# Performance work log

Hardware: AMD Instinct MI355X
Metric: run time of the kernel (lower is better)

The kernel has to match this reference:

```python
import jax, jax.numpy as jnp
import numpy as np

N_NODES = 20000; N_EDGES = 200000
FN = 128; FE = 64; D = 128; T = 128; K = 5
H = 4; DH = D // H; N_LAYERS = 2; FF = 4 * D
B = 32768
T0 = 0.0; EPS = 1e-5


def _ln(x, s, b):
    m = jnp.mean(x, axis=-1, keepdims=True)
    v = jnp.mean(jnp.square(x - m), axis=-1, keepdims=True)
    return (x - m) / jnp.sqrt(v + EPS) * s + b


def setup_inputs() -> dict:
    key = jax.random.key(0)
    ks = jax.random.split(key, 24)
    def w(i, shape, s=0.05):
        return jax.random.normal(ks[i], shape, jnp.float32) * s
    return {
        "src": jax.random.randint(ks[0], (B,), 0, N_NODES),
        "dst": jax.random.randint(ks[1], (B,), 0, N_NODES),
        "neg": jax.random.randint(ks[2], (B,), 0, N_NODES),
        "eidx": jax.random.randint(ks[3], (B,), 0, N_EDGES),
        "ts": jax.random.uniform(ks[4], (B,), jnp.float32) * 1000.0,
        "node_feats": w(5, (N_NODES, FN), 1.0),
        "edge_feats": w(6, (N_EDGES, FE), 1.0),
        "node_lin_w": w(7, (D, FN)), "node_lin_b": jnp.zeros((D,), jnp.float32),
        "edge_lin_w": w(8, (D, FE)), "edge_lin_b": jnp.zeros((D,), jnp.float32),
        "time_w": w(9, (T,), 1.0), "time_b": w(10, (T,), 1.0),
        "tok_w": w(11, (D, 3 * D + T)), "tok_b": jnp.zeros((D,), jnp.float32),
        "qkv_w": w(12, (N_LAYERS, 3 * D, D)), "qkv_b": jnp.zeros((N_LAYERS, 3 * D), jnp.float32),
        "attn_w": w(13, (N_LAYERS, D, D)), "attn_b": jnp.zeros((N_LAYERS, D), jnp.float32),
        "ln1_s": jnp.ones((N_LAYERS, D), jnp.float32), "ln1_b": jnp.zeros((N_LAYERS, D), jnp.float32),
        "ln2_s": jnp.ones((N_LAYERS, D), jnp.float32), "ln2_b": jnp.zeros((N_LAYERS, D), jnp.float32),
        "ff1_w": w(14, (N_LAYERS, FF, D)), "ff1_b": jnp.zeros((N_LAYERS, FF), jnp.float32),
        "ff2_w": w(15, (N_LAYERS, D, FF)), "ff2_b": jnp.zeros((N_LAYERS, D), jnp.float32),
        "p1_w": w(16, (D, D)), "p1_b": jnp.zeros((D,), jnp.float32),
        "p2_w": w(17, (K, D)), "p2_b": jnp.zeros((K,), jnp.float32),
    }


def reference(src, dst, neg, eidx, ts, node_feats, edge_feats,
              node_lin_w, node_lin_b, edge_lin_w, edge_lin_b,
              time_w, time_b, tok_w, tok_b,
              qkv_w, qkv_b, attn_w, attn_b,
              ln1_s, ln1_b, ln2_s, ln2_b,
              ff1_w, ff1_b, ff2_w, ff2_b,
              p1_w, p1_b, p2_w, p2_b):
    # --- occurrence tokens: [src occs | dst occs | neg occs] = 3B tokens ---
    self_nodes = jnp.concatenate([src, dst, neg])          # [3B]
    other_nodes = jnp.concatenate([dst, src, src])         # [3B]
    eidx_all = jnp.concatenate([eidx, eidx, eidx])
    ts_all = jnp.concatenate([ts, ts, ts])
    Ntot = self_nodes.shape[0]

    base_self = node_feats[self_nodes] @ node_lin_w.T + node_lin_b    # [3B, D]
    base_other = node_feats[other_nodes] @ node_lin_w.T + node_lin_b
    edge_emb = edge_feats[eidx_all] @ edge_lin_w.T + edge_lin_b       # [3B, D]
    time_emb = jnp.cos((ts_all - T0)[:, None] * time_w[None, :] + time_b)  # [3B, T]
    x_cat = jnp.concatenate([base_self, base_other, edge_emb, time_emb], axis=-1)
    tok = jax.nn.relu(x_cat @ tok_w.T + tok_b)                        # [3B, D]

    # --- group occurrences by node, sort by time, pad (device-side) ---
    node_ids = jnp.unique(self_nodes)                      # [Nn]
    order = jnp.lexsort((ts_all, self_nodes))              # primary node, secondary time
    nodes_s = self_nodes[order]
    row_s = jnp.searchsorted(node_ids, nodes_s)            # row per sorted occ
    starts = jnp.searchsorted(nodes_s, node_ids)           # start of each group
    pos_s = jnp.arange(Ntot) - starts[row_s]               # pos within group
    node_row = jnp.zeros((Ntot,), jnp.int32).at[order].set(row_s.astype(jnp.int32))
    pos_map = jnp.zeros((Ntot,), jnp.int32).at[order].set(pos_s.astype(jnp.int32))
    seq_len = jnp.diff(jnp.concatenate([starts, jnp.array([Ntot], starts.dtype)]))
    Nn = int(node_ids.shape[0])
    Lmax = int(seq_len.max())

    x_pad = jnp.zeros((Nn, Lmax, D), tok.dtype).at[node_row, pos_map].set(tok)
    pad_mask = jnp.arange(Lmax)[None, :] >= seq_len[:, None]  # True = padded key

    # --- pre-LN TransformerEncoder (gelu, no final norm) ---
    scale = jnp.float32(1.0 / np.sqrt(DH))
    x = x_pad
    for l in range(N_LAYERS):
        h = _ln(x, ln1_s[l], ln1_b[l])
        qkv = h @ qkv_w[l].T + qkv_b[l]                    # [Nn, L, 3D]
        q, k, v = jnp.split(qkv, 3, axis=-1)
        q = q.reshape(Nn, Lmax, H, DH); k = k.reshape(Nn, Lmax, H, DH); v = v.reshape(Nn, Lmax, H, DH)
        scores = jnp.einsum('nqhd,nkhd->nhqk', q, k) * scale
        scores = jnp.where(pad_mask[:, None, None, :], jnp.float32(-1e9), scores)
        a = jax.nn.softmax(scores, axis=-1)
        o = jnp.einsum('nhqk,nkhd->nqhd', a, v).reshape(Nn, Lmax, D)
        x = x + o @ attn_w[l].T + attn_b[l]
        h2 = _ln(x, ln2_s[l], ln2_b[l])
        x = x + jax.nn.gelu(h2 @ ff1_w[l].T + ff1_b[l], approximate=False) @ ff2_w[l].T + ff2_b[l]

    # --- gather per-occurrence outputs and project to community probs ---
    def proj(hh):
        return jax.nn.softmax(jax.nn.relu(hh @ p1_w.T + p1_b) @ p2_w.T + p2_b, axis=-1)
    src_h = x[node_row[:B], pos_map[:B]]
    dst_h = x[node_row[B:2 * B], pos_map[B:2 * B]]
    neg_h = x[node_row[2 * B:], pos_map[2 * B:]]
    return proj(src_h), proj(dst_h), proj(neg_h)
```

## Files before the change

kernel.cpp:

```cpp
#include <hip/hip_runtime.h>
#include <hip/hip_bf16.h>
#include <math.h>

#define NB 32768
#define NTOK (3 * NB)
#define NNODES 20000
#define MAXL 64

typedef short bf16x8 __attribute__((ext_vector_type(8)));
typedef float f32x4 __attribute__((ext_vector_type(4)));

typedef __attribute__((address_space(3))) void lds_t;
typedef const __attribute__((address_space(1))) void gbl_t;

__device__ __forceinline__ float b2f(short s) {
    unsigned int u = ((unsigned int)(unsigned short)s) << 16;
    union { unsigned int u; float f; } c;
    c.u = u;
    return c.f;
}


__global__ void convert_k(const float* __restrict__ in, __hip_bfloat16* __restrict__ out, int n) {
    int i = blockIdx.x * 256 + threadIdx.x;
    int stride = gridDim.x * 256;
    for (; i < n; i += stride) out[i] = __float2bfloat16(in[i]);
}

__global__ void fold12_k(const float* __restrict__ tok_w, const float* __restrict__ nl_w,
                         __hip_bfloat16* __restrict__ A12) {
    int idx = blockIdx.x * 256 + threadIdx.x;
    if (idx >= 256 * 128) return;
    int n = idx >> 7, f = idx & 127;
    const float* tw = (n < 128) ? (tok_w + n * 512) : (tok_w + (n - 128) * 512 + 128);
    float acc = 0.f;
    for (int c = 0; c < 128; ++c) acc += tw[c] * nl_w[c * 128 + f];
    A12[idx] = __float2bfloat16(acc);
}

__global__ void foldE_k(const float* __restrict__ tok_w, const float* __restrict__ el_w,
                        __hip_bfloat16* __restrict__ AE) {
    int idx = blockIdx.x * 256 + threadIdx.x;
    if (idx >= 128 * 192) return;
    int d = idx / 192, j = idx % 192;
    float acc;
    if (j < 64) {
        acc = 0.f;
        for (int c = 0; c < 128; ++c) acc += tok_w[d * 512 + 256 + c] * el_w[c * 64 + j];
    } else {
        acc = tok_w[d * 512 + 384 + (j - 64)];
    }
    AE[idx] = __float2bfloat16(acc);
}

__global__ void foldb_k(const float* __restrict__ tok_w, const float* __restrict__ tok_b,
                        const float* __restrict__ nl_b, const float* __restrict__ el_b,
                        float* __restrict__ bf) {
    int d = threadIdx.x;
    if (d >= 128) return;
    float acc = tok_b[d];
    for (int c = 0; c < 128; ++c)
        acc += (tok_w[d * 512 + c] + tok_w[d * 512 + 128 + c]) * nl_b[c];
    for (int c = 0; c < 128; ++c)
        acc += tok_w[d * 512 + 256 + c] * el_b[c];
    bf[d] = acc;
}

__device__ __forceinline__ int self_node(int t, const int* src, const int* dst, const int* neg) {
    if (t < NB) return src[t];
    if (t < 2 * NB) return dst[t - NB];
    return neg[t - 2 * NB];
}

__global__ void count_k(const int* __restrict__ src, const int* __restrict__ dst,
                        const int* __restrict__ neg, int* __restrict__ cnt) {
    int t = blockIdx.x * 256 + threadIdx.x;
    if (t >= NTOK) return;
    atomicAdd(&cnt[self_node(t, src, dst, neg)], 1);
}

__global__ __launch_bounds__(1024) void scan_k(const int* __restrict__ cnt,
                                               int* __restrict__ starts) {
    __shared__ int ps[1024];
    int t = threadIdx.x;
    const int PER = 20;
    int base = t * PER;
    int loc[PER];
    int s = 0;
#pragma unroll
    for (int k = 0; k < PER; ++k) {
        int i = base + k;
        int v = (i < NNODES) ? cnt[i] : 0;
        loc[k] = s;
        s += v;
    }
    ps[t] = s;
    __syncthreads();
    for (int off = 1; off < 1024; off <<= 1) {
        int v = (t >= off) ? ps[t - off] : 0;
        __syncthreads();
        ps[t] += v;
        __syncthreads();
    }
    int offv = (t > 0) ? ps[t - 1] : 0;
#pragma unroll
    for (int k = 0; k < PER; ++k) {
        int i = base + k;
        if (i < NNODES) starts[i] = offv + loc[k];
    }
}

__global__ void scatter_k(const int* __restrict__ src, const int* __restrict__ dst,
                          const int* __restrict__ neg, const int* __restrict__ starts,
                          int* __restrict__ cursor, int* __restrict__ order) {
    int t = blockIdx.x * 256 + threadIdx.x;
    if (t >= NTOK) return;
    int node = self_node(t, src, dst, neg);
    int p = atomicAdd(&cursor[node], 1);
    order[starts[node] + p] = t;
}

__global__ void aemb_k(const int* __restrict__ eidx, const float* __restrict__ ts,
                       const float* __restrict__ ef, const float* __restrict__ tw,
                       const float* __restrict__ tb, __hip_bfloat16* __restrict__ Aemb) {
    int idx = blockIdx.x * 256 + threadIdx.x;
    if (idx >= NB * 192) return;
    int m = idx / 192, j = idx % 192;
    float v;
    if (j < 64) v = ef[(size_t)eidx[m] * 64 + j];
    else { int c = j - 64; v = cosf(ts[m] * tw[c] + tb[c]); }
    Aemb[idx] = __float2bfloat16(v);
}

__global__ __launch_bounds__(256) void asm_emb_k(
    const int* __restrict__ order, const int* __restrict__ src, const int* __restrict__ dst,
    const int* __restrict__ neg, const float* __restrict__ P12, const float* __restrict__ E,
    const float* __restrict__ s, const float* __restrict__ b,
    float* __restrict__ x, __hip_bfloat16* __restrict__ h) {
    int p = blockIdx.x * 4 + (threadIdx.x >> 6);
    int lane = threadIdx.x & 63;
    int t = order[p];
    int m, self, other;
    if (t < NB) { m = t; self = src[m]; other = dst[m]; }
    else if (t < 2 * NB) { m = t - NB; self = dst[m]; other = src[m]; }
    else { m = t - 2 * NB; self = neg[m]; other = src[m]; }
    int d0 = lane, d1 = lane + 64;
    float v0 = P12[(size_t)self * 256 + d0] + P12[(size_t)other * 256 + 128 + d0] +
               E[(size_t)m * 128 + d0];
    float v1 = P12[(size_t)self * 256 + d1] + P12[(size_t)other * 256 + 128 + d1] +
               E[(size_t)m * 128 + d1];
    v0 = fmaxf(v0, 0.f);
    v1 = fmaxf(v1, 0.f);
    float sum = v0 + v1;
#pragma unroll
    for (int off = 32; off; off >>= 1) sum += __shfl_xor(sum, off, 64);
    float mean = sum * (1.f / 128.f);
    float c0 = v0 - mean, c1 = v1 - mean;
    float vs = c0 * c0 + c1 * c1;
#pragma unroll
    for (int off = 32; off; off >>= 1) vs += __shfl_xor(vs, off, 64);
    float inv = rsqrtf(vs * (1.f / 128.f) + 1e-5f);
    x[(size_t)p * 128 + d0] = v0;
    x[(size_t)p * 128 + d1] = v1;
    h[(size_t)p * 128 + d0] = __float2bfloat16(c0 * inv * s[d0] + b[d0]);
    h[(size_t)p * 128 + d1] = __float2bfloat16(c1 * inv * s[d1] + b[d1]);
}

__device__ __forceinline__ float gelu_f(float v) {
    float ax = fabsf(v) * 0.70710678118654752f;
    float t = 1.f / (1.f + 0.3275911f * ax);
    float poly = ((((1.061405429f * t - 1.453152027f) * t + 1.421413741f) * t -
                   0.284496736f) * t + 0.254829592f) * t;
    float erf_ax = 1.f - poly * __expf(-ax * ax);
    float erfv = (v < 0.f) ? -erf_ax : erf_ax;
    return 0.5f * v * (1.f + erfv);
}

__global__ __launch_bounds__(256) void gemm_k(
    const __hip_bfloat16* __restrict__ A, const __hip_bfloat16* __restrict__ B,
    const float* __restrict__ bias, float* __restrict__ Cf, int M, int N, int K) {
    __shared__ float4 As4[1024];
    __shared__ float4 Bs4[1024];
    int tid = threadIdx.x;
    int lane = tid & 63, wid = tid >> 6;
    int wm = wid & 1, wn = wid >> 1;
    int mBase = blockIdx.x * 128, nBase = blockIdx.y * 128;
    const float4 fzero = {0.f, 0.f, 0.f, 0.f};
    f32x4 acc[4][4];
#pragma unroll
    for (int i = 0; i < 4; ++i)
#pragma unroll
        for (int j = 0; j < 4; ++j) {
            f32x4 z = {0.f, 0.f, 0.f, 0.f};
            acc[i][j] = z;
        }
    bf16x8* AsV = reinterpret_cast<bf16x8*>(As4);
    bf16x8* BsV = reinterpret_cast<bf16x8*>(Bs4);

    for (int k0 = 0; k0 < K; k0 += 64) {
#pragma unroll
        for (int i = 0; i < 4; ++i) {
            int cid = i * 256 + tid;
            int r = cid >> 3, c = cid & 7;
            int sidx = r * 8 + (c ^ (r & 7));
            int gr = mBase + r;
            float4 va = fzero;
            if (gr < M)
                va = *reinterpret_cast<const float4*>(A + (size_t)gr * K + k0 + c * 8);
            As4[sidx] = va;
            int gn = nBase + r;
            Bs4[sidx] = *reinterpret_cast<const float4*>(B + (size_t)gn * K + k0 + c * 8);
        }
        __syncthreads();
#pragma unroll
        for (int kk = 0; kk < 2; ++kk) {
            bf16x8 a[4], b[4];
            int ccol = kk * 4 + (lane >> 4);
#pragma unroll
            for (int f = 0; f < 4; ++f) {
                int ra = wm * 64 + f * 16 + (lane & 15);
                a[f] = AsV[ra * 8 + (ccol ^ (ra & 7))];
                int rb = wn * 64 + f * 16 + (lane & 15);
                b[f] = BsV[rb * 8 + (ccol ^ (rb & 7))];
            }
#pragma unroll
            for (int fm = 0; fm < 4; ++fm)
#pragma unroll
                for (int fn = 0; fn < 4; ++fn)
                    acc[fm][fn] = __builtin_amdgcn_mfma_f32_16x16x32_bf16(
                        a[fm], b[fn], acc[fm][fn], 0, 0, 0);
        }
        __syncthreads();
    }

    int colBase = nBase + wn * 64;
#pragma unroll
    for (int fm = 0; fm < 4; ++fm) {
        int row0 = mBase + wm * 64 + fm * 16 + (lane >> 4) * 4;
#pragma unroll
        for (int fn = 0; fn < 4; ++fn) {
            int col = colBase + fn * 16 + (lane & 15);
            float bv = bias ? bias[col] : 0.f;
#pragma unroll
            for (int j = 0; j < 4; ++j) {
                int row = row0 + j;
                if (row >= M) continue;
                Cf[(size_t)row * N + col] = acc[fm][fn][j] + bv;
            }
        }
    }
}

#define G2_BF16 0
#define G2_GELU 1
#define G2_ADD_LN 2
#define G2_ADD_BF16 3

template <int MODE>
__global__ __launch_bounds__(256) void gemm3_k(
    const __hip_bfloat16* __restrict__ A, const __hip_bfloat16* __restrict__ B,
    const float* __restrict__ bias, float* __restrict__ x,
    const float* __restrict__ lns, const float* __restrict__ lnb,
    __hip_bfloat16* __restrict__ hout, int N) {
    __shared__ __align__(16) __hip_bfloat16 sA[128 * 128];
    __shared__ __align__(16) __hip_bfloat16 sB[128 * 128];
    __shared__ float redS[2][128];
    __shared__ float redS2[2][128];
    int tid = threadIdx.x;
    int lane = tid & 63, wid = tid >> 6;
    int wm = wid & 1, wn = wid >> 1;
    int mBase = blockIdx.x * 128, nBase = blockIdx.y * 128;
    f32x4 acc[4][4];
#pragma unroll
    for (int i = 0; i < 4; ++i)
#pragma unroll
        for (int j = 0; j < 4; ++j) {
            f32x4 z = {0.f, 0.f, 0.f, 0.f};
            acc[i][j] = z;
        }

#pragma unroll
    for (int i = 0; i < 8; ++i) {
        int cid = i * 256 + tid;
        int row = cid >> 4, slotS = cid & 15;
        int slotG = slotS ^ (row & 15);
        const __hip_bfloat16* ga = A + (size_t)(mBase + row) * 128 + slotG * 8;
        const __hip_bfloat16* gb = B + (size_t)(nBase + row) * 128 + slotG * 8;
        __builtin_amdgcn_global_load_lds((gbl_t*)ga, (lds_t*)&sA[(cid & ~63) * 8], 16, 0, 0);
        __builtin_amdgcn_global_load_lds((gbl_t*)gb, (lds_t*)&sB[(cid & ~63) * 8], 16, 0, 0);
    }
    asm volatile("s_waitcnt vmcnt(0)" ::: "memory");
    __builtin_amdgcn_s_barrier();
    __builtin_amdgcn_sched_barrier(0);

    const bf16x8* AsV = reinterpret_cast<const bf16x8*>(sA);
    const bf16x8* BsV = reinterpret_cast<const bf16x8*>(sB);
#pragma unroll
    for (int kk = 0; kk < 4; ++kk) {
        bf16x8 a[4], b[4];
        int kvec = kk * 4 + (lane >> 4);
#pragma unroll
        for (int f = 0; f < 4; ++f) {
            int ra = wm * 64 + f * 16 + (lane & 15);
            a[f] = AsV[ra * 16 + (kvec ^ (ra & 15))];
            int rb = wn * 64 + f * 16 + (lane & 15);
            b[f] = BsV[rb * 16 + (kvec ^ (rb & 15))];
        }
#pragma unroll
        for (int fm = 0; fm < 4; ++fm)
#pragma unroll
            for (int fn = 0; fn < 4; ++fn)
                acc[fm][fn] = __builtin_amdgcn_mfma_f32_16x16x32_bf16(
                    a[fm], b[fn], acc[fm][fn], 0, 0, 0);
    }

    if (MODE == G2_BF16 || MODE == G2_GELU) {
        int colBase = nBase + wn * 64;
#pragma unroll
        for (int fm = 0; fm < 4; ++fm) {
            int row0 = mBase + wm * 64 + fm * 16 + (lane >> 4) * 4;
#pragma unroll
            for (int fn = 0; fn < 4; ++fn) {
                int col = colBase + fn * 16 + (lane & 15);
                float bv = bias[col];
#pragma unroll
                for (int j = 0; j < 4; ++j) {
                    float v = acc[fm][fn][j] + bv;
                    if (MODE == G2_GELU) v = gelu_f(v);
                    hout[(size_t)(row0 + j) * N + col] = __float2bfloat16(v);
                }
            }
        }
    } else {
#pragma unroll
        for (int fm = 0; fm < 4; ++fm) {
            int rl0 = wm * 64 + fm * 16 + (lane >> 4) * 4;
#pragma unroll
            for (int fn = 0; fn < 4; ++fn) {
                int col = wn * 64 + fn * 16 + (lane & 15);
                float bv = bias[col];
#pragma unroll
                for (int j = 0; j < 4; ++j) {
                    size_t off = (size_t)(mBase + rl0 + j) * 128 + col;
                    float v = acc[fm][fn][j] + bv + x[off];
                    x[off] = v;
                    acc[fm][fn][j] = v;
                }
            }
        }
        if (MODE == G2_ADD_BF16) {
#pragma unroll
            for (int fm = 0; fm < 4; ++fm) {
                int rl0 = wm * 64 + fm * 16 + (lane >> 4) * 4;
#pragma unroll
                for (int fn = 0; fn < 4; ++fn) {
                    int col = wn * 64 + fn * 16 + (lane & 15);
#pragma unroll
                    for (int j = 0; j < 4; ++j)
                        hout[(size_t)(mBase + rl0 + j) * 128 + col] =
                            __float2bfloat16(acc[fm][fn][j]);
                }
            }
        } else {
#pragma unroll
            for (int fm = 0; fm < 4; ++fm) {
#pragma unroll
                for (int j = 0; j < 4; ++j) {
                    float s1 = 0.f, s2 = 0.f;
#pragma unroll
                    for (int fn = 0; fn < 4; ++fn) {
                        float v = acc[fm][fn][j];
                        s1 += v;
                        s2 += v * v;
                    }
#pragma unroll
                    for (int off = 1; off < 16; off <<= 1) {
                        s1 += __shfl_xor(s1, off, 64);
                        s2 += __shfl_xor(s2, off, 64);
                    }
                    if ((lane & 15) == 0) {
                        int rl = wm * 64 + fm * 16 + (lane >> 4) * 4 + j;
                        redS[wn][rl] = s1;
                        redS2[wn][rl] = s2;
                    }
                }
            }
            __syncthreads();
#pragma unroll
            for (int fm = 0; fm < 4; ++fm) {
                int rl0 = wm * 64 + fm * 16 + (lane >> 4) * 4;
#pragma unroll
                for (int j = 0; j < 4; ++j) {
                    int rl = rl0 + j;
                    float mean = (redS[0][rl] + redS[1][rl]) * (1.f / 128.f);
                    float var = (redS2[0][rl] + redS2[1][rl]) * (1.f / 128.f) - mean * mean;
                    float inv = rsqrtf(var + 1e-5f);
#pragma unroll
                    for (int fn = 0; fn < 4; ++fn) {
                        int col = wn * 64 + fn * 16 + (lane & 15);
                        float c = (acc[fm][fn][j] - mean) * inv;
                        hout[(size_t)(mBase + rl) * 128 + col] =
                            __float2bfloat16(c * lns[col] + lnb[col]);
                    }
                }
            }
        }
    }
}

template <int MODE>
__global__ __launch_bounds__(256) void gemm2_k(
    const __hip_bfloat16* __restrict__ A, const __hip_bfloat16* __restrict__ B,
    const float* __restrict__ bias, float* __restrict__ x,
    const float* __restrict__ lns, const float* __restrict__ lnb,
    __hip_bfloat16* __restrict__ hout, int N, int K) {
    __shared__ __align__(16) __hip_bfloat16 sA[2][128 * 64];
    __shared__ __align__(16) __hip_bfloat16 sB[2][128 * 64];
    __shared__ float redS[2][128];
    __shared__ float redS2[2][128];
    int tid = threadIdx.x;
    int lane = tid & 63, wid = tid >> 6;
    int wm = wid & 1, wn = wid >> 1;
    int mBase = blockIdx.x * 128, nBase = blockIdx.y * 128;
    f32x4 acc[4][4];
#pragma unroll
    for (int i = 0; i < 4; ++i)
#pragma unroll
        for (int j = 0; j < 4; ++j) {
            f32x4 z = {0.f, 0.f, 0.f, 0.f};
            acc[i][j] = z;
        }

    auto stage = [&](int buf, int k0) {
#pragma unroll
        for (int i = 0; i < 4; ++i) {
            int cid = i * 256 + tid;
            int row = cid >> 3, slotS = cid & 7;
            int slotG = slotS ^ (row & 7);
            const __hip_bfloat16* ga = A + (size_t)(mBase + row) * K + k0 + slotG * 8;
            const __hip_bfloat16* gb = B + (size_t)(nBase + row) * K + k0 + slotG * 8;
            __hip_bfloat16* la = &sA[buf][(cid & ~63) * 8];
            __hip_bfloat16* lb = &sB[buf][(cid & ~63) * 8];
            __builtin_amdgcn_global_load_lds((gbl_t*)ga, (lds_t*)la, 16, 0, 0);
            __builtin_amdgcn_global_load_lds((gbl_t*)gb, (lds_t*)lb, 16, 0, 0);
        }
    };

    int nt = K >> 6;
    stage(0, 0);
    int cur = 0;
    for (int t = 0; t < nt; ++t) {
        if (t + 1 < nt) {
            stage(cur ^ 1, (t + 1) << 6);
            asm volatile("s_waitcnt vmcnt(8)" ::: "memory");
        } else {
            asm volatile("s_waitcnt vmcnt(0)" ::: "memory");
        }
        __builtin_amdgcn_s_barrier();
        __builtin_amdgcn_sched_barrier(0);
        const bf16x8* AsV = reinterpret_cast<const bf16x8*>(sA[cur]);
        const bf16x8* BsV = reinterpret_cast<const bf16x8*>(sB[cur]);
#pragma unroll
        for (int kk = 0; kk < 2; ++kk) {
            bf16x8 a[4], b[4];
            int kvec = kk * 4 + (lane >> 4);
#pragma unroll
            for (int f = 0; f < 4; ++f) {
                int ra = wm * 64 + f * 16 + (lane & 15);
                a[f] = AsV[ra * 8 + (kvec ^ (ra & 7))];
                int rb = wn * 64 + f * 16 + (lane & 15);
                b[f] = BsV[rb * 8 + (kvec ^ (rb & 7))];
            }
#pragma unroll
            for (int fm = 0; fm < 4; ++fm)
#pragma unroll
                for (int fn = 0; fn < 4; ++fn)
                    acc[fm][fn] = __builtin_amdgcn_mfma_f32_16x16x32_bf16(
                        a[fm], b[fn], acc[fm][fn], 0, 0, 0);
        }
        __builtin_amdgcn_s_barrier();
        cur ^= 1;
    }

#pragma unroll
    for (int fm = 0; fm < 4; ++fm) {
        int rl0 = wm * 64 + fm * 16 + (lane >> 4) * 4;
#pragma unroll
        for (int fn = 0; fn < 4; ++fn) {
            int col = wn * 64 + fn * 16 + (lane & 15);
            float bv = bias[col];
#pragma unroll
            for (int j = 0; j < 4; ++j) {
                size_t off = (size_t)(mBase + rl0 + j) * 128 + col;
                float v = acc[fm][fn][j] + bv + x[off];
                x[off] = v;
                acc[fm][fn][j] = v;
            }
        }
    }
    if (MODE == G2_ADD_BF16) {
#pragma unroll
        for (int fm = 0; fm < 4; ++fm) {
            int rl0 = wm * 64 + fm * 16 + (lane >> 4) * 4;
#pragma unroll
            for (int fn = 0; fn < 4; ++fn) {
                int col = wn * 64 + fn * 16 + (lane & 15);
#pragma unroll
                for (int j = 0; j < 4; ++j)
                    hout[(size_t)(mBase + rl0 + j) * 128 + col] =
                        __float2bfloat16(acc[fm][fn][j]);
            }
        }
    } else {
#pragma unroll
        for (int fm = 0; fm < 4; ++fm) {
#pragma unroll
            for (int j = 0; j < 4; ++j) {
                float s1 = 0.f, s2 = 0.f;
#pragma unroll
                for (int fn = 0; fn < 4; ++fn) {
                    float v = acc[fm][fn][j];
                    s1 += v;
                    s2 += v * v;
                }
#pragma unroll
                for (int off = 1; off < 16; off <<= 1) {
                    s1 += __shfl_xor(s1, off, 64);
                    s2 += __shfl_xor(s2, off, 64);
                }
                if ((lane & 15) == 0) {
                    int rl = wm * 64 + fm * 16 + (lane >> 4) * 4 + j;
                    redS[wn][rl] = s1;
                    redS2[wn][rl] = s2;
                }
            }
        }
        __syncthreads();
#pragma unroll
        for (int fm = 0; fm < 4; ++fm) {
            int rl0 = wm * 64 + fm * 16 + (lane >> 4) * 4;
#pragma unroll
            for (int j = 0; j < 4; ++j) {
                int rl = rl0 + j;
                float mean = (redS[0][rl] + redS[1][rl]) * (1.f / 128.f);
                float var = (redS2[0][rl] + redS2[1][rl]) * (1.f / 128.f) - mean * mean;
                float inv = rsqrtf(var + 1e-5f);
#pragma unroll
                for (int fn = 0; fn < 4; ++fn) {
                    int col = wn * 64 + fn * 16 + (lane & 15);
                    float c = (acc[fm][fn][j] - mean) * inv;
                    hout[(size_t)(mBase + rl) * 128 + col] =
                        __float2bfloat16(c * lns[col] + lnb[col]);
                }
            }
        }
    }
}

__global__ __launch_bounds__(256) void attn_k(
    const __hip_bfloat16* __restrict__ qkv, const int* __restrict__ starts,
    const int* __restrict__ cnt, __hip_bfloat16* __restrict__ o) {
    __shared__ float sc[4][4][4][MAXL];
    int wid = threadIdx.x >> 6, lane = threadIdx.x & 63;
    int node = blockIdx.x * 4 + wid;
    if (node >= NNODES) return;
    int st = starts[node];
    int len = cnt[node];
    if (len <= 0) return;
    if (len > MAXL) len = MAXL;
    int qs = lane >> 4, li = lane & 15, h = li >> 2;
    const float scale = 0.17677669529663687f;

    for (int qb = 0; qb < len; qb += 4) {
        int qi = qb + qs;
        bool act = qi < len;
        int qidx = act ? qi : len - 1;
        bf16x8 qv = *reinterpret_cast<const bf16x8*>(
            qkv + (size_t)(st + qidx) * 384 + li * 8);
        float qf[8];
#pragma unroll
        for (int e = 0; e < 8; ++e) qf[e] = b2f(qv[e]);
        for (int j = 0; j < len; ++j) {
            bf16x8 kv = *reinterpret_cast<const bf16x8*>(
                qkv + (size_t)(st + j) * 384 + 128 + li * 8);
            float d = 0.f;
#pragma unroll
            for (int e = 0; e < 8; ++e) d += qf[e] * b2f(kv[e]);
            d += __shfl_xor(d, 1, 64);
            d += __shfl_xor(d, 2, 64);
            if ((li & 3) == 0) sc[wid][qs][h][j] = d * scale;
        }
        float mx = -1e30f;
        for (int j = li & 3; j < len; j += 4) mx = fmaxf(mx, sc[wid][qs][h][j]);
        mx = fmaxf(mx, __shfl_xor(mx, 1, 64));
        mx = fmaxf(mx, __shfl_xor(mx, 2, 64));
        float ssum = 0.f;
        for (int j = li & 3; j < len; j += 4) {
            float e = __expf(sc[wid][qs][h][j] - mx);
            sc[wid][qs][h][j] = e;
            ssum += e;
        }
        ssum += __shfl_xor(ssum, 1, 64);
        ssum += __shfl_xor(ssum, 2, 64);
        float sinv = 1.f / ssum;
        float accv[8] = {0.f, 0.f, 0.f, 0.f, 0.f, 0.f, 0.f, 0.f};
        for (int j = 0; j < len; ++j) {
            float p = sc[wid][qs][h][j];
            bf16x8 vv = *reinterpret_cast<const bf16x8*>(
                qkv + (size_t)(st + j) * 384 + 256 + li * 8);
#pragma unroll
            for (int e = 0; e < 8; ++e) accv[e] += p * b2f(vv[e]);
        }
        if (act) {
            bf16x8 ov;
#pragma unroll
            for (int e = 0; e < 8; ++e) {
                __hip_bfloat16 t = __float2bfloat16(accv[e] * sinv);
                ov[e] = *reinterpret_cast<short*>(&t);
            }
            *reinterpret_cast<bf16x8*>(o + (size_t)(st + qi) * 128 + li * 8) = ov;
        }
    }
}

__global__ __launch_bounds__(256) void p1head_k(
    const __hip_bfloat16* __restrict__ A, const __hip_bfloat16* __restrict__ B,
    const float* __restrict__ bias, const float* __restrict__ p2w,
    const float* __restrict__ p2b, const int* __restrict__ order,
    float* __restrict__ out) {
    __shared__ __align__(16) char smem[65536];
    __shared__ float p2s[640];
    __shared__ float p2bs[5];
    float4* As4 = (float4*)smem;
    float4* Bs4 = (float4*)(smem + 16384);
    float* rowbuf = (float*)smem;
    int tid = threadIdx.x;
    for (int i = tid; i < 640; i += 256) p2s[i] = p2w[i];
    if (tid < 5) p2bs[tid] = p2b[tid];
    int lane = tid & 63, wid = tid >> 6;
    int wm = wid & 1, wn = wid >> 1;
    int mBase = blockIdx.x * 128;
    f32x4 acc[4][4];
#pragma unroll
    for (int i = 0; i < 4; ++i)
#pragma unroll
        for (int j = 0; j < 4; ++j) {
            f32x4 z = {0.f, 0.f, 0.f, 0.f};
            acc[i][j] = z;
        }
    bf16x8* AsV = reinterpret_cast<bf16x8*>(As4);
    bf16x8* BsV = reinterpret_cast<bf16x8*>(Bs4);
    for (int k0 = 0; k0 < 128; k0 += 64) {
#pragma unroll
        for (int i = 0; i < 4; ++i) {
            int cid = i * 256 + tid;
            int r = cid >> 3, c = cid & 7;
            int sidx = r * 8 + (c ^ (r & 7));
            As4[sidx] = *reinterpret_cast<const float4*>(A + (size_t)(mBase + r) * 128 + k0 + c * 8);
            Bs4[sidx] = *reinterpret_cast<const float4*>(B + (size_t)r * 128 + k0 + c * 8);
        }
        __syncthreads();
#pragma unroll
        for (int kk = 0; kk < 2; ++kk) {
            bf16x8 a[4], bb[4];
            int ccol = kk * 4 + (lane >> 4);
#pragma unroll
            for (int f = 0; f < 4; ++f) {
                int ra = wm * 64 + f * 16 + (lane & 15);
                a[f] = AsV[ra * 8 + (ccol ^ (ra & 7))];
                int rb = wn * 64 + f * 16 + (lane & 15);
                bb[f] = BsV[rb * 8 + (ccol ^ (rb & 7))];
            }
#pragma unroll
            for (int fm = 0; fm < 4; ++fm)
#pragma unroll
                for (int fn = 0; fn < 4; ++fn)
                    acc[fm][fn] = __builtin_amdgcn_mfma_f32_16x16x32_bf16(
                        a[fm], bb[fn], acc[fm][fn], 0, 0, 0);
        }
        __syncthreads();
    }
#pragma unroll
    for (int fm = 0; fm < 4; ++fm) {
        int rl0 = wm * 64 + fm * 16 + (lane >> 4) * 4;
#pragma unroll
        for (int fn = 0; fn < 4; ++fn) {
            int col = wn * 64 + fn * 16 + (lane & 15);
            float bv = bias[col];
#pragma unroll
            for (int j = 0; j < 4; ++j) {
                int rl = rl0 + j;
                rowbuf[rl * 128 + (col ^ ((rl & 7) << 2))] = fmaxf(acc[fm][fn][j] + bv, 0.f);
            }
        }
    }
    __syncthreads();
    int row = tid >> 1, half = tid & 1;
    int swz = (row & 7) << 2;
    float lg[5] = {0.f, 0.f, 0.f, 0.f, 0.f};
    for (int i = 0; i < 64; ++i) {
        int col = half * 64 + i;
        float rv = rowbuf[row * 128 + (col ^ swz)];
#pragma unroll
        for (int k = 0; k < 5; ++k) lg[k] += rv * p2s[k * 128 + col];
    }
#pragma unroll
    for (int k = 0; k < 5; ++k) lg[k] += __shfl_xor(lg[k], 1, 64);
    if (half == 0) {
        float mx = -1e30f;
#pragma unroll
        for (int k = 0; k < 5; ++k) {
            lg[k] += p2bs[k];
            mx = fmaxf(mx, lg[k]);
        }
        float e[5], ssum = 0.f;
#pragma unroll
        for (int k = 0; k < 5; ++k) {
            e[k] = __expf(lg[k] - mx);
            ssum += e[k];
        }
        float si = 1.f / ssum;
        int t = order[mBase + row];
#pragma unroll
        for (int k = 0; k < 5; ++k) out[(size_t)t * 5 + k] = e[k] * si;
    }
}


extern "C" void kernel_launch(void* const* d_in, const int* in_sizes, int n_in,
                              void* d_out, int out_size, void* d_ws, size_t ws_size,
                              hipStream_t stream) {
    const int* src = (const int*)d_in[0];
    const int* dst = (const int*)d_in[1];
    const int* neg = (const int*)d_in[2];
    const int* eidx = (const int*)d_in[3];
    const float* ts = (const float*)d_in[4];
    const float* node_feats = (const float*)d_in[5];
    const float* edge_feats = (const float*)d_in[6];
    const float* node_lin_w = (const float*)d_in[7];
    const float* node_lin_b = (const float*)d_in[8];
    const float* edge_lin_w = (const float*)d_in[9];
    const float* edge_lin_b = (const float*)d_in[10];
    const float* time_w = (const float*)d_in[11];
    const float* time_b = (const float*)d_in[12];
    const float* tok_w = (const float*)d_in[13];
    const float* tok_b = (const float*)d_in[14];
    const float* qkv_w = (const float*)d_in[15];
    const float* qkv_b = (const float*)d_in[16];
    const float* attn_w = (const float*)d_in[17];
    const float* attn_b = (const float*)d_in[18];
    const float* ln1_s = (const float*)d_in[19];
    const float* ln1_b = (const float*)d_in[20];
    const float* ln2_s = (const float*)d_in[21];
    const float* ln2_b = (const float*)d_in[22];
    const float* ff1_w = (const float*)d_in[23];
    const float* ff1_b = (const float*)d_in[24];
    const float* ff2_w = (const float*)d_in[25];
    const float* ff2_b = (const float*)d_in[26];
    const float* p1_w = (const float*)d_in[27];
    const float* p1_b = (const float*)d_in[28];
    const float* p2_w = (const float*)d_in[29];
    const float* p2_b = (const float*)d_in[30];
    float* out = (float*)d_out;

    char* w = (char*)d_ws;
    auto alloc = [&](size_t bytes) {
        char* p = w;
        w += (bytes + 255) & ~(size_t)255;
        return p;
    };
    float* x = (float*)alloc((size_t)NTOK * 128 * 4);
    __hip_bfloat16* h = (__hip_bfloat16*)alloc((size_t)NTOK * 128 * 2);
    char* big = alloc((size_t)(NTOK + 64) * 512 * 2);
    __hip_bfloat16* qkvb = (__hip_bfloat16*)big;
    __hip_bfloat16* ob = (__hip_bfloat16*)(big + (size_t)(NTOK + 64) * 384 * 2);
    __hip_bfloat16* ub = (__hip_bfloat16*)big;
    float* P12 = (float*)alloc((size_t)NNODES * 256 * 4);
    float* E = (float*)alloc((size_t)NB * 128 * 4);
    __hip_bfloat16* Aemb = (__hip_bfloat16*)alloc((size_t)NB * 192 * 2);
    __hip_bfloat16* nfb = (__hip_bfloat16*)alloc((size_t)NNODES * 128 * 2);
    __hip_bfloat16* A12 = (__hip_bfloat16*)alloc(256 * 128 * 2);
    __hip_bfloat16* AE = (__hip_bfloat16*)alloc(128 * 192 * 2);
    float* bfold = (float*)alloc(128 * 4);
    __hip_bfloat16* qkvwb = (__hip_bfloat16*)alloc(2 * 384 * 128 * 2);
    __hip_bfloat16* attnwb = (__hip_bfloat16*)alloc(2 * 128 * 128 * 2);
    __hip_bfloat16* ff1wb = (__hip_bfloat16*)alloc(2 * 512 * 128 * 2);
    __hip_bfloat16* ff2wb = (__hip_bfloat16*)alloc(2 * 128 * 512 * 2);
    __hip_bfloat16* p1wb = (__hip_bfloat16*)alloc(128 * 128 * 2);
    int* cnt = (int*)alloc(NNODES * 4);
    int* starts = (int*)alloc(NNODES * 4);
    int* cursor = (int*)alloc(NNODES * 4);
    int* order = (int*)alloc(NTOK * 4);

    hipMemsetAsync(cnt, 0, NNODES * 4, stream);
    hipMemsetAsync(cursor, 0, NNODES * 4, stream);

    auto cvt = [&](const float* in, __hip_bfloat16* outp, int n) {
        int blocks = (n + 255) / 256;
        if (blocks > 2048) blocks = 2048;
        convert_k<<<blocks, 256, 0, stream>>>(in, outp, n);
    };
    cvt(node_feats, nfb, NNODES * 128);
    cvt(qkv_w, qkvwb, 2 * 384 * 128);
    cvt(attn_w, attnwb, 2 * 128 * 128);
    cvt(ff1_w, ff1wb, 2 * 512 * 128);
    cvt(ff2_w, ff2wb, 2 * 128 * 512);
    cvt(p1_w, p1wb, 128 * 128);

    fold12_k<<<128, 256, 0, stream>>>(tok_w, node_lin_w, A12);
    foldE_k<<<96, 256, 0, stream>>>(tok_w, edge_lin_w, AE);
    foldb_k<<<1, 128, 0, stream>>>(tok_w, tok_b, node_lin_b, edge_lin_b, bfold);

    count_k<<<(NTOK + 255) / 256, 256, 0, stream>>>(src, dst, neg, cnt);
    scan_k<<<1, 1024, 0, stream>>>(cnt, starts);
    scatter_k<<<(NTOK + 255) / 256, 256, 0, stream>>>(src, dst, neg, starts, cursor, order);

    aemb_k<<<(NB * 192 + 255) / 256, 256, 0, stream>>>(eidx, ts, edge_feats, time_w, time_b, Aemb);

    gemm_k<<<dim3(157, 2), 256, 0, stream>>>(nfb, A12, nullptr, P12, NNODES, 256, 128);
    gemm_k<<<dim3(256, 1), 256, 0, stream>>>(Aemb, AE, bfold, E, NB, 128, 192);
    asm_emb_k<<<NTOK / 4, 256, 0, stream>>>(order, src, dst, neg, P12, E,
                                            ln1_s, ln1_b, x, h);

    const int gm = NTOK / 128;
    for (int l = 0; l < 2; ++l) {
        gemm3_k<G2_BF16><<<dim3(gm, 3), 256, 0, stream>>>(
            h, qkvwb + (size_t)l * 384 * 128, qkv_b + l * 384,
            nullptr, nullptr, nullptr, qkvb, 384);
        attn_k<<<(NNODES + 3) / 4, 256, 0, stream>>>(qkvb, starts, cnt, ob);
        gemm3_k<G2_ADD_LN><<<dim3(gm, 1), 256, 0, stream>>>(
            ob, attnwb + (size_t)l * 128 * 128, attn_b + l * 128,
            x, ln2_s + l * 128, ln2_b + l * 128, h, 128);
        gemm3_k<G2_GELU><<<dim3(gm, 4), 256, 0, stream>>>(
            h, ff1wb + (size_t)l * 512 * 128, ff1_b + l * 512,
            nullptr, nullptr, nullptr, ub, 512);
        if (l == 0)
            gemm2_k<G2_ADD_LN><<<dim3(gm, 1), 256, 0, stream>>>(
                ub, ff2wb, ff2_b, x, ln1_s + 128, ln1_b + 128, h, 128, 512);
        else
            gemm2_k<G2_ADD_BF16><<<dim3(gm, 1), 256, 0, stream>>>(
                ub, ff2wb + (size_t)128 * 512, ff2_b + 128, x,
                nullptr, nullptr, h, 128, 512);
    }

    p1head_k<<<gm, 256, 0, stream>>>(h, p1wb, p1_b, p2_w, p2_b, order, out);
}
```

Baseline: 627.5 us.

## Add A-resident GEMM that streams B in double-buffered 64-column chunks

Adds a gemm4_k kernel that loads the 128x128 A tile into LDS once per block and then loops over all N output columns in 64-wide chunks, double-buffering the B chunks with async global-to-LDS loads. It replaces the N-split grid launches for the node projection, QKV and FF1 GEMMs, so each A tile is read once instead of once per column block. The node feature buffer is padded by 128 rows because the new kernel reads the A tile without a bounds check. The cost is fewer blocks, which lowers parallelism, and a serial loop over chunks per block.

```diff
diff --git a/kernel.cpp b/kernel.cpp
--- a/kernel.cpp
+++ b/kernel.cpp
@@ -255,6 +255,107 @@
 #define G2_GELU 1
 #define G2_ADD_LN 2
 #define G2_ADD_BF16 3
+#define G4_F32 4
+
+template <int MODE>
+__global__ __launch_bounds__(256) void gemm4_k(
+    const __hip_bfloat16* __restrict__ A, const __hip_bfloat16* __restrict__ B,
+    const float* __restrict__ bias, float* __restrict__ Cf,
+    __hip_bfloat16* __restrict__ Cb, int M, int N) {
+    __shared__ __align__(16) __hip_bfloat16 sA[128 * 128];
+    __shared__ __align__(16) __hip_bfloat16 sB[2][64 * 128];
+    int tid = threadIdx.x;
+    int lane = tid & 63, wid = tid >> 6;
+    int wm = wid & 1, wn = wid >> 1;
+    int mBase = blockIdx.x * 128;
+
+#pragma unroll
+    for (int i = 0; i < 8; ++i) {
+        int cid = i * 256 + tid;
+        int row = cid >> 4, slotS = cid & 15;
+        int slotG = slotS ^ (row & 15);
+        const __hip_bfloat16* ga = A + (size_t)(mBase + row) * 128 + slotG * 8;
+        __builtin_amdgcn_global_load_lds((gbl_t*)ga, (lds_t*)&sA[(cid & ~63) * 8], 16, 0, 0);
+    }
+    auto stageB = [&](int buf, int c) {
+#pragma unroll
+        for (int i = 0; i < 4; ++i) {
+            int cid = i * 256 + tid;
+            int row = cid >> 4, slotS = cid & 15;
+            int slotG = slotS ^ (row & 15);
+            const __hip_bfloat16* gb = B + (size_t)(c * 64 + row) * 128 + slotG * 8;
+            __builtin_amdgcn_global_load_lds((gbl_t*)gb, (lds_t*)&sB[buf][(cid & ~63) * 8],
+                                             16, 0, 0);
+        }
+    };
+    int nc = N >> 6;
+    stageB(0, 0);
+    const bf16x8* AsV = reinterpret_cast<const bf16x8*>(sA);
+
+    for (int c = 0; c < nc; ++c) {
+        if (c + 1 < nc) {
+            stageB((c + 1) & 1, c + 1);
+            asm volatile("s_waitcnt vmcnt(4)" ::: "memory");
+        } else {
+            asm volatile("s_waitcnt vmcnt(0)" ::: "memory");
+        }
+        __builtin_amdgcn_s_barrier();
+        __builtin_amdgcn_sched_barrier(0);
+        const bf16x8* BsV = reinterpret_cast<const bf16x8*>(sB[c & 1]);
+        f32x4 acc[4][2];
+#pragma unroll
+        for (int i = 0; i < 4; ++i)
+#pragma unroll
+            for (int j = 0; j < 2; ++j) {
+                f32x4 z = {0.f, 0.f, 0.f, 0.f};
+                acc[i][j] = z;
+            }
+#pragma unroll
+        for (int kk = 0; kk < 4; ++kk) {
+            int kvec = kk * 4 + (lane >> 4);
+            bf16x8 a[4], b[2];
+#pragma unroll
+            for (int f = 0; f < 4; ++f) {
+                int ra = wm * 64 + f * 16 + (lane & 15);
+                a[f] = AsV[ra * 16 + (kvec ^ (ra & 15))];
+            }
+#pragma unroll
+            for (int f = 0; f < 2; ++f) {
+                int rb = wn * 32 + f * 16 + (lane & 15);
+                b[f] = BsV[rb * 16 + (kvec ^ (rb & 15))];
+            }
+#pragma unroll
+            for (int fm = 0; fm < 4; ++fm)
+#pragma unroll
+                for (int fn = 0; fn < 2; ++fn)
+                    acc[fm][fn] = __builtin_amdgcn_mfma_f32_16x16x32_bf16(
+                        a[fm], b[fn], acc[fm][fn], 0, 0, 0);
+        }
+        __builtin_amdgcn_s_barrier();
+        int colC = c * 64 + wn * 32;
+#pragma unroll
+        for (int fm = 0; fm < 4; ++fm) {
+            int row0 = mBase + wm * 64 + fm * 16 + (lane >> 4) * 4;
+#pragma unroll
+            for (int fn = 0; fn < 2; ++fn) {
+                int col = colC + fn * 16 + (lane & 15);
+                float bv = bias ? bias[col] : 0.f;
+#pragma unroll
+                for (int j = 0; j < 4; ++j) {
+                    int row = row0 + j;
+                    float v = acc[fm][fn][j] + bv;
+                    if (MODE == G4_F32) {
+                        if (row < M) Cf[(size_t)row * N + col] = v;
+                    } else if (MODE == G2_GELU) {
+                        Cb[(size_t)row * N + col] = __float2bfloat16(gelu_f(v));
+                    } else {
+                        Cb[(size_t)row * N + col] = __float2bfloat16(v);
+                    }
+                }
+            }
+        }
+    }
+}
 
 template <int MODE>
 __global__ __launch_bounds__(256) void gemm3_k(
@@ -778,7 +879,7 @@
     float* P12 = (float*)alloc((size_t)NNODES * 256 * 4);
     float* E = (float*)alloc((size_t)NB * 128 * 4);
     __hip_bfloat16* Aemb = (__hip_bfloat16*)alloc((size_t)NB * 192 * 2);
-    __hip_bfloat16* nfb = (__hip_bfloat16*)alloc((size_t)NNODES * 128 * 2);
+    __hip_bfloat16* nfb = (__hip_bfloat16*)alloc((size_t)(NNODES + 128) * 128 * 2);
     __hip_bfloat16* A12 = (__hip_bfloat16*)alloc(256 * 128 * 2);
     __hip_bfloat16* AE = (__hip_bfloat16*)alloc(128 * 192 * 2);
     float* bfold = (float*)alloc(128 * 4);
@@ -817,23 +918,23 @@
 
     aemb_k<<<(NB * 192 + 255) / 256, 256, 0, stream>>>(eidx, ts, edge_feats, time_w, time_b, Aemb);
 
-    gemm_k<<<dim3(157, 2), 256, 0, stream>>>(nfb, A12, nullptr, P12, NNODES, 256, 128);
+    gemm4_k<G4_F32><<<157, 256, 0, stream>>>(nfb, A12, nullptr, P12, nullptr, NNODES, 256);
     gemm_k<<<dim3(256, 1), 256, 0, stream>>>(Aemb, AE, bfold, E, NB, 128, 192);
     asm_emb_k<<<NTOK / 4, 256, 0, stream>>>(order, src, dst, neg, P12, E,
                                             ln1_s, ln1_b, x, h);
 
     const int gm = NTOK / 128;
     for (int l = 0; l < 2; ++l) {
-        gemm3_k<G2_BF16><<<dim3(gm, 3), 256, 0, stream>>>(
+        gemm4_k<G2_BF16><<<gm, 256, 0, stream>>>(
             h, qkvwb + (size_t)l * 384 * 128, qkv_b + l * 384,
-            nullptr, nullptr, nullptr, qkvb, 384);
+            nullptr, qkvb, NTOK, 384);
         attn_k<<<(NNODES + 3) / 4, 256, 0, stream>>>(qkvb, starts, cnt, ob);
         gemm3_k<G2_ADD_LN><<<dim3(gm, 1), 256, 0, stream>>>(
             ob, attnwb + (size_t)l * 128 * 128, attn_b + l * 128,
             x, ln2_s + l * 128, ln2_b + l * 128, h, 128);
-        gemm3_k<G2_GELU><<<dim3(gm, 4), 256, 0, stream>>>(
+        gemm4_k<G2_GELU><<<gm, 256, 0, stream>>>(
             h, ff1wb + (size_t)l * 512 * 128, ff1_b + l * 512,
-            nullptr, nullptr, nullptr, ub, 512);
+            nullptr, ub, NTOK, 512);
         if (l == 0)
             gemm2_k<G2_ADD_LN><<<dim3(gm, 1), 256, 0, stream>>>(
                 ub, ff2wb, ff2_b, x, ln1_s + 128, ln1_b + 128, h, 128, 512);
```

After: 686.2 us. 9.4% more time.
